# Kernel tuning notes

Hardware: AMD Instinct MI355X
Metric: run time of the kernel (lower is better)

Reference implementation:

```python
import jax, jax.numpy as jnp
import numpy as np

N, E, D, T = 50000, 800000, 64, 4
FI = D // T   # per-tower input features (divide_input=True)
FO = D // T   # per-tower output features (output_dim // towers)
NAGG, NSC = 4, 3  # mean/min/max/std ; identity/amplification/attenuation
AVG_LOG = float(np.log(17.0))  # from deg histogram: all nodes have degree 16


def setup_inputs() -> dict:
    key = jax.random.key(0)
    ks = jax.random.split(key, 12)
    rn = lambda k, s: jax.random.normal(k, s, dtype=jnp.float32) * 0.1
    z = lambda s: jnp.zeros(s, jnp.float32)
    post_in = (1 + NAGG * NSC) * FI  # cat([x, scaled aggregations]) per tower
    return {
        "x": jax.random.normal(ks[0], (N, D), dtype=jnp.float32),
        "edge_index": jax.random.randint(ks[1], (2, E), 0, N),
        "alpha": jnp.full((1,), 0.5, dtype=jnp.float32),
        "lin_self_W": rn(ks[2], (D, D)), "lin_self_b": z((D,)),
        "pre_W_s2d": rn(ks[3], (T, 2 * FI, FI)), "pre_b_s2d": z((T, FI)),
        "post_W_s2d": rn(ks[4], (T, post_in, FO)), "post_b_s2d": z((T, FO)),
        "lin_W_s2d": rn(ks[5], (T * FO, D)), "lin_b_s2d": z((D,)),
        "pre_W_d2s": rn(ks[6], (T, 2 * FI, FI)), "pre_b_d2s": z((T, FI)),
        "post_W_d2s": rn(ks[7], (T, post_in, FO)), "post_b_d2s": z((T, FO)),
        "lin_W_d2s": rn(ks[8], (T * FO, D)), "lin_b_d2s": z((D,)),
    }


def _pna(x, recv, send, preW, preb, postW, postb, linW, linb):
    """One PNAConv: messages from `send` nodes aggregated at `recv` nodes."""
    n = x.shape[0]
    xt = x.reshape(n, T, FI)
    # message: per tower cat(x_i, x_j) -> single pre layer (pre_layers=1)
    h = jnp.concatenate([xt[recv], xt[send]], axis=-1)          # [E, T, 2*FI]
    m = jnp.einsum('etf,tfg->etg', h, preW) + preb              # [E, T, FI]
    # aggregators: mean, min, max, std (scatter-reduce over receiver)
    cnt = jax.ops.segment_sum(jnp.ones((recv.shape[0],), m.dtype), recv, n)
    deg = jnp.maximum(cnt, 1.0)[:, None, None]                  # clamp(1), as PyG
    mean = jax.ops.segment_sum(m, recv, n) / deg
    mean_sq = jax.ops.segment_sum(m * m, recv, n) / deg
    std = jnp.sqrt(jnp.maximum(mean_sq - mean * mean, 0.0) + 1e-5)
    has = (cnt > 0.0)[:, None, None]
    mn = jnp.where(has, jax.ops.segment_min(m, recv, n), 0.0)
    mx = jnp.where(has, jax.ops.segment_max(m, recv, n), 0.0)
    agg = jnp.concatenate([mean, mn, mx, std], axis=-1)         # [n, T, 4*FI]
    # degree scalers: identity, amplification, attenuation
    amp = jnp.log(deg + 1.0) / AVG_LOG
    out = jnp.concatenate([agg, agg * amp, agg / amp], axis=-1)  # [n, T, 12*FI]
    out = jnp.concatenate([xt, out], axis=-1)                   # [n, T, 13*FI]
    out = jnp.einsum('ntf,tfg->ntg', out, postW) + postb        # [n, T, FO]
    return out.reshape(n, T * FO) @ linW + linb                 # [n, D]


def reference(x, edge_index, alpha, lin_self_W, lin_self_b,
              pre_W_s2d, pre_b_s2d, post_W_s2d, post_b_s2d, lin_W_s2d, lin_b_s2d,
              pre_W_d2s, pre_b_d2s, post_W_d2s, post_b_d2s, lin_W_d2s, lin_b_d2s):
    src, dst = edge_index[0], edge_index[1]
    y_self = x @ lin_self_W + lin_self_b
    # flow='source_to_target': x_j = src, aggregated at dst
    y_s2d = _pna(x, dst, src, pre_W_s2d, pre_b_s2d, post_W_s2d, post_b_s2d, lin_W_s2d, lin_b_s2d)
    # flow='target_to_source': x_j = dst, aggregated at src
    y_d2s = _pna(x, src, dst, pre_W_d2s, pre_b_d2s, post_W_d2s, post_b_d2s, lin_W_d2s, lin_b_d2s)
    a = alpha[0]
    return y_self + (1.0 - a) * y_s2d + a * y_d2s
```

## Files before the change

kernel.cpp:

```cpp
#include <hip/hip_runtime.h>
#include <math.h>


typedef _Float16 half_t;
typedef __attribute__((ext_vector_type(8))) _Float16 half8;
typedef __attribute__((ext_vector_type(2))) _Float16 half2v;
typedef __attribute__((ext_vector_type(4))) float f32x4;

#define FCAP 12288

static __device__ __forceinline__ unsigned pkmin(unsigned a, unsigned b) {
    unsigned r;
    asm("v_pk_min_f16 %0, %1, %2" : "=v"(r) : "v"(a), "v"(b));
    return r;
}
static __device__ __forceinline__ unsigned pkmax(unsigned a, unsigned b) {
    unsigned r;
    asm("v_pk_max_f16 %0, %1, %2" : "=v"(r) : "v"(a), "v"(b));
    return r;
}
static __device__ __forceinline__ int h2i(half2v h) { return __builtin_bit_cast(int, h); }
static __device__ __forceinline__ half2v i2h(int i) { return __builtin_bit_cast(half2v, i); }
static __device__ __forceinline__ half2v u2h(unsigned i) { return __builtin_bit_cast(half2v, i); }
static __device__ __forceinline__ half2v pkrtz(float a, float b) {
    return __builtin_bit_cast(half2v, __builtin_amdgcn_cvt_pkrtz(a, b));
}

__global__ __launch_bounds__(256) void k_pre(
    const int* __restrict__ ei, int nE, int nN,
    int* __restrict__ histD, int* __restrict__ histS,
    const float* __restrict__ postW1, const float* __restrict__ postW2,
    const float* __restrict__ linW1, const float* __restrict__ linW2,
    const float* __restrict__ Wself, const float* __restrict__ bself,
    const float* __restrict__ linb1, const float* __restrict__ linb2,
    const float* __restrict__ postb1, const float* __restrict__ postb2,
    const float* __restrict__ alpha,
    half_t* __restrict__ WLg, half_t* __restrict__ WfinTg, float* __restrict__ bfin,
    const float* __restrict__ x,
    const float* __restrict__ preW1, const float* __restrict__ preW2,
    const float* __restrict__ preb1, const float* __restrict__ preb2,
    half_t* __restrict__ P1, half_t* __restrict__ P2,
    half_t* __restrict__ Q1, half_t* __restrict__ Q2, half_t* __restrict__ xh) {
    int tid = threadIdx.x;
    int b = blockIdx.x;
    if (b < 256) {
        __shared__ int hD[256], hS[256];
        hD[tid] = 0; hS[tid] = 0;
        __syncthreads();
        int chunk = (nE + 255) >> 8;
        int lo = b * chunk;
        int hi = lo + chunk; if (hi > nE) hi = nE;
        for (int e = lo + tid; e < hi; e += 256) {
            int s = ei[e], d = ei[nE + e];
            atomicAdd(&hD[d >> 8], 1);
            atomicAdd(&hS[s >> 8], 1);
        }
        __syncthreads();
        histD[tid * 256 + b] = hD[tid];
        histS[tid * 256 + b] = hS[tid];
    } else if (b < 320) {
        const float a = alpha[0];
        int id = (b - 256) * 256 + tid;
        const int stride = 64 * 256;
        for (int i = id; i < 24 * 16 * 72; i += stride) {
            int m = i / (16 * 72);
            int r = i % (16 * 72);
            int go = r / 72, k = r % 72;
            int d = m / 12, t = (m / 3) % 4, mat = m % 3;
            float v = 0.f;
            if (k < 64) {
                int stat = k >> 4, g = k & 15;
                int basep = (mat == 0) ? 1 : (mat == 1 ? 5 : 9);
                const float* pw = d ? postW2 : postW1;
                v = pw[t * 3328 + ((basep + stat) * 16 + g) * 16 + go];
            }
            WLg[i] = (half_t)v;
        }
        for (int i = id; i < 64 * 192; i += stride) {
            int o = i / 192, k = i % 192;
            float v;
            if (k < 64)       v = (1.f - a) * linW1[k * 64 + o];
            else if (k < 128) v = a * linW2[(k - 64) * 64 + o];
            else {
                int kx = k - 128, t = kx >> 4, f = kx & 15;
                v = Wself[kx * 64 + o];
                float s1 = 0.f, s2 = 0.f;
                for (int go = 0; go < 16; ++go) {
                    s1 += postW1[t * 3328 + f * 16 + go] * linW1[(t * 16 + go) * 64 + o];
                    s2 += postW2[t * 3328 + f * 16 + go] * linW2[(t * 16 + go) * 64 + o];
                }
                v += (1.f - a) * s1 + a * s2;
            }
            WfinTg[i] = (half_t)v;
        }
        for (int i = id; i < 64; i += stride) {
            float v = bself[i] + (1.f - a) * linb1[i] + a * linb2[i];
            for (int j = 0; j < 64; ++j)
                v += (1.f - a) * postb1[j] * linW1[j * 64 + i]
                   + a * postb2[j] * linW2[j * 64 + i];
            bfin[i] = v;
        }
    } else {
        int vb = b - 320;
        const int lane = tid & 63;
        const int t = lane >> 4, g = lane & 15;
        const int base = t << 4;
        float wsP1[16], wsP2[16], wsQ1[16], wsQ2[16];
#pragma unroll
        for (int f = 0; f < 16; ++f) {
            wsP1[f] = preW1[t * 512 + (16 + f) * 16 + g];
            wsP2[f] = preW2[t * 512 + (16 + f) * 16 + g];
            wsQ1[f] = preW1[t * 512 + f * 16 + g];
            wsQ2[f] = preW2[t * 512 + f * 16 + g];
        }
        const float pb1 = preb1[lane], pb2 = preb2[lane];
        int node = (vb * 256 + tid) >> 6;
        const int stride = (768 * 256) >> 6;
        for (; node < nN; node += stride) {
            float xv = x[(size_t)node * 64 + lane];
            float p1 = 0.f, p2 = 0.f, q1 = pb1, q2 = pb2;
#pragma unroll
            for (int f = 0; f < 16; ++f) {
                float v = __shfl(xv, base + f, 64);
                p1 = fmaf(v, wsP1[f], p1);
                p2 = fmaf(v, wsP2[f], p2);
                q1 = fmaf(v, wsQ1[f], q1);
                q2 = fmaf(v, wsQ2[f], q2);
            }
            size_t o = (size_t)node * 64 + lane;
            P1[o] = (half_t)p1;
            P2[o] = (half_t)p2;
            Q1[o] = (half_t)q1;
            Q2[o] = (half_t)q2;
            xh[o] = (half_t)xv;
        }
    }
}

__global__ __launch_bounds__(256) void k_scanA(
    const int* __restrict__ cnt0, const int* __restrict__ cnt1,
    int* __restrict__ off0, int* __restrict__ off1,
    int* __restrict__ bsum, int n, int nchunk) {
    int arr = blockIdx.x >= nchunk;
    int c = blockIdx.x - (arr ? nchunk : 0);
    const int* cnt = arr ? cnt1 : cnt0;
    int* off = arr ? off1 : off0;
    int tid = threadIdx.x;
    int base = c * 1024 + tid * 4;
    int v[4];
#pragma unroll
    for (int k = 0; k < 4; ++k) { int i = base + k; v[k] = (i < n) ? cnt[i] : 0; }
    int tsum = v[0] + v[1] + v[2] + v[3];
    int lane = tid & 63, wid = tid >> 6;
    int incl = tsum;
#pragma unroll
    for (int d = 1; d < 64; d <<= 1) {
        int t = __shfl_up(incl, d, 64);
        if (lane >= d) incl += t;
    }
    __shared__ int ws[4];
    if (lane == 63) ws[wid] = incl;
    __syncthreads();
    int wpre = 0;
    for (int ww = 0; ww < wid; ++ww) wpre += ws[ww];
    int e = wpre + incl - tsum;
#pragma unroll
    for (int k = 0; k < 4; ++k) { int i = base + k; if (i < n) off[i] = e; e += v[k]; }
    if (tid == 255) bsum[blockIdx.x] = wpre + incl;
}

__global__ __launch_bounds__(256) void k_scanB(
    int* __restrict__ off0, int* __restrict__ off1,
    const int* __restrict__ bsum, int n, int nchunk) {
    int arr = blockIdx.x >= nchunk;
    int c = blockIdx.x - (arr ? nchunk : 0);
    int* off = arr ? off1 : off0;
    const int* bs = bsum + (arr ? nchunk : 0);
    __shared__ int pre_s, tot_s;
    int tid = threadIdx.x;
    if (tid < 64) {
        int v = (tid < nchunk) ? bs[tid] : 0;
        int incl = v;
#pragma unroll
        for (int d = 1; d < 64; d <<= 1) {
            int t = __shfl_up(incl, d, 64);
            if (tid >= d) incl += t;
        }
        if (tid == c) pre_s = incl - v;
        if (tid == nchunk - 1) tot_s = incl;
    }
    __syncthreads();
    int pre = pre_s;
    int base = c * 1024 + tid * 4;
#pragma unroll
    for (int k = 0; k < 4; ++k) {
        int i = base + k;
        if (i < n) off[i] += pre;
    }
    if (c == 0 && tid == 0) off[n] = tot_s;
}

__global__ __launch_bounds__(256) void k_bin(
    const int* __restrict__ ei, int nE, int nbuck,
    const int* __restrict__ curD, const int* __restrict__ curS,
    unsigned* __restrict__ binnedD, unsigned* __restrict__ binnedS) {
    __shared__ int cD[256], cS[256];
    int tid = threadIdx.x;
    int hb = blockIdx.x;
    if (tid < nbuck) {
        cD[tid] = curD[tid * 256 + hb];
        cS[tid] = curS[tid * 256 + hb];
    }
    __syncthreads();
    int chunk = (nE + 255) >> 8;
    int lo = hb * chunk;
    int hi = lo + chunk; if (hi > nE) hi = nE;
    for (int e = lo + tid; e < hi; e += 256) {
        int s = ei[e], d = ei[nE + e];
        unsigned pk = (unsigned)s | ((unsigned)d << 16);
        int p = atomicAdd(&cD[d >> 8], 1);
        binnedD[p] = pk;
        int q = atomicAdd(&cS[s >> 8], 1);
        binnedS[q] = pk;
    }
}

__global__ __launch_bounds__(256) void k_fine(
    const unsigned* __restrict__ binnedD, const unsigned* __restrict__ binnedS,
    const int* __restrict__ curD, const int* __restrict__ curS,
    int* __restrict__ off_dst, int* __restrict__ off_src,
    unsigned short* __restrict__ adj_dst, unsigned short* __restrict__ adj_src,
    int nE, int nN, int nbuck) {
    int bk = blockIdx.x;
    int dd = 0;
    if (bk >= nbuck) { dd = 1; bk -= nbuck; }
    const unsigned* binned = dd ? binnedS : binnedD;
    const int* cur = dd ? curS : curD;
    int* off = dd ? off_src : off_dst;
    unsigned short* adj = dd ? adj_src : adj_dst;
    __shared__ int ncnt[256];
    __shared__ int cur2[256];
    __shared__ unsigned short stage[FCAP];
    int tid = threadIdx.x;
    ncnt[tid] = 0;
    __syncthreads();
    int base = cur[bk * 256];
    int endp = cur[(bk + 1) * 256];
    int cntE = endp - base;
    int n0 = bk << 8;
    for (int i = tid; i < cntE; i += 256) {
        unsigned pk = binned[base + i];
        int key = dd ? (int)(pk & 0xFFFFu) : (int)(pk >> 16);
        atomicAdd(&ncnt[key - n0], 1);
    }
    __syncthreads();
    if (tid < 64) {
        int i4 = tid << 2;
        int v0 = ncnt[i4], v1 = ncnt[i4 + 1], v2 = ncnt[i4 + 2], v3 = ncnt[i4 + 3];
        int tsum = v0 + v1 + v2 + v3;
        int incl = tsum;
#pragma unroll
        for (int d = 1; d < 64; d <<= 1) {
            int t = __shfl_up(incl, d, 64);
            if (tid >= d) incl += t;
        }
        int excl = incl - tsum;
        ncnt[i4] = excl;
        ncnt[i4 + 1] = excl + v0;
        ncnt[i4 + 2] = excl + v0 + v1;
        ncnt[i4 + 3] = excl + v0 + v1 + v2;
    }
    __syncthreads();
    cur2[tid] = ncnt[tid];
    int node = n0 + tid;
    if (node < nN) off[node] = base + ncnt[tid];
    if (bk == nbuck - 1 && tid == 0) off[nN] = nE;
    __syncthreads();
    for (int i = tid; i < cntE; i += 256) {
        unsigned pk = binned[base + i];
        int key = dd ? (int)(pk & 0xFFFFu) : (int)(pk >> 16);
        int oth = dd ? (int)(pk >> 16) : (int)(pk & 0xFFFFu);
        int pos = atomicAdd(&cur2[key - n0], 1);
        if (pos < FCAP) stage[pos] = (unsigned short)oth;
        else adj[base + pos] = (unsigned short)oth;
    }
    __syncthreads();
    int lim = cntE < FCAP ? cntE : FCAP;
    for (int i = tid; i < lim; i += 256) adj[base + i] = stage[i];
}

__global__ __launch_bounds__(256) void k_gather(
    const half_t* __restrict__ P1, const half_t* __restrict__ P2,
    const half_t* __restrict__ Q1, const half_t* __restrict__ Q2,
    const int* __restrict__ off1, const unsigned short* __restrict__ adj1,
    const int* __restrict__ off2, const unsigned short* __restrict__ adj2,
    half_t* __restrict__ agg1, half_t* __restrict__ agg2,
    float* __restrict__ amp1, float* __restrict__ ramp1,
    float* __restrict__ amp2, float* __restrict__ ramp2, int nN, int nE) {
    int tid = threadIdx.x;
    const int lane = tid & 63;
    const int grp = lane >> 4;
    const int fl = lane & 15;
    const int fl8 = fl << 3;
    int wstart = (blockIdx.x * blockDim.x + tid) >> 6;
    int wstride = (gridDim.x * blockDim.x) >> 6;
#pragma unroll
    for (int d = 0; d < 2; ++d) {
        const char* Pc = (const char*)(d ? P2 : P1);
        const char* Qc = (const char*)(d ? Q2 : Q1);
        const int* off = d ? off2 : off1;
        const unsigned short* adj = d ? adj2 : adj1;
        char* aggc = (char*)(d ? agg2 : agg1);
        float* ampA = d ? amp2 : amp1;
        float* rampA = d ? ramp2 : ramp1;
        for (int node = wstart; node < nN; node += wstride) {
            int beg = off[node], end = off[node + 1];
            int cnt = end - beg;
            int li = beg + lane;
            int adjv = adj[li < nE ? li : 0];
            half2v s01 = {(half_t)0, (half_t)0}, s23 = {(half_t)0, (half_t)0};
            half2v ss01 = {(half_t)0, (half_t)0}, ss23 = {(half_t)0, (half_t)0};
            unsigned mn0 = 0x7C007C00u, mn1 = 0x7C007C00u;
            unsigned mx0 = 0xFC00FC00u, mx1 = 0xFC00FC00u;
            int jm = (cnt < 64) ? (cnt & ~7) : 64;
            int j = 0;
            for (; j + 8 <= jm; j += 8) {
                int na = __shfl(adjv, j + grp, 64);
                int nb = __shfl(adjv, j + 4 + grp, 64);
                uint2 ua = *(const uint2*)(Pc + na * 128 + fl8);
                uint2 ub = *(const uint2*)(Pc + nb * 128 + fl8);
                half2v a0 = u2h(ua.x), a1 = u2h(ua.y);
                half2v b0 = u2h(ub.x), b1 = u2h(ub.y);
                s01 += a0 + b0; s23 += a1 + b1;
                ss01 += a0 * a0; ss23 += a1 * a1;
                ss01 += b0 * b0; ss23 += b1 * b1;
                mn0 = pkmin(mn0, pkmin(ua.x, ub.x));
                mn1 = pkmin(mn1, pkmin(ua.y, ub.y));
                mx0 = pkmax(mx0, pkmax(ua.x, ub.x));
                mx1 = pkmax(mx1, pkmax(ua.y, ub.y));
            }
            for (int jj = beg + j; jj < end; jj += 4) {
                int idx = jj + grp;
                if (idx < end) {
                    int nc = adj[idx];
                    uint2 uc = *(const uint2*)(Pc + nc * 128 + fl8);
                    half2v c0 = u2h(uc.x), c1 = u2h(uc.y);
                    s01 += c0; s23 += c1;
                    ss01 += c0 * c0; ss23 += c1 * c1;
                    mn0 = pkmin(mn0, uc.x); mn1 = pkmin(mn1, uc.y);
                    mx0 = pkmax(mx0, uc.x); mx1 = pkmax(mx1, uc.y);
                }
            }
#pragma unroll
            for (int sh = 16; sh <= 32; sh <<= 1) {
                s01 += i2h(__shfl_xor(h2i(s01), sh, 64));
                s23 += i2h(__shfl_xor(h2i(s23), sh, 64));
                ss01 += i2h(__shfl_xor(h2i(ss01), sh, 64));
                ss23 += i2h(__shfl_xor(h2i(ss23), sh, 64));
                mn0 = pkmin(mn0, (unsigned)__shfl_xor((int)mn0, sh, 64));
                mn1 = pkmin(mn1, (unsigned)__shfl_xor((int)mn1, sh, 64));
                mx0 = pkmax(mx0, (unsigned)__shfl_xor((int)mx0, sh, 64));
                mx1 = pkmax(mx1, (unsigned)__shfl_xor((int)mx1, sh, 64));
            }
            float deg = (cnt > 0) ? (float)cnt : 1.0f;
            float inv = 1.0f / deg;
            float se0 = (float)s01[0], se1 = (float)s01[1];
            float se2 = (float)s23[0], se3 = (float)s23[1];
            float sq0 = (float)ss01[0], sq1 = (float)ss01[1];
            float sq2 = (float)ss23[0], sq3 = (float)ss23[1];
            float me0 = se0 * inv, me1 = se1 * inv, me2 = se2 * inv, me3 = se3 * inv;
            float st0 = sqrtf(fmaxf(fmaf(-me0, me0, sq0 * inv), 0.f) + 1e-5f);
            float st1 = sqrtf(fmaxf(fmaf(-me1, me1, sq1 * inv), 0.f) + 1e-5f);
            float st2 = sqrtf(fmaxf(fmaf(-me2, me2, sq2 * inv), 0.f) + 1e-5f);
            float st3 = sqrtf(fmaxf(fmaf(-me3, me3, sq3 * inv), 0.f) + 1e-5f);
            uint2 qu = *(const uint2*)(Qc + node * 128 + fl8);
            half2v q01 = u2h(qu.x), q23 = u2h(qu.y);
            half2v hm01, hm23, hl01, hl23, hh01, hh23;
            if (cnt > 0) {
                hm01 = q01 + pkrtz(me0, me1);
                hm23 = q23 + pkrtz(me2, me3);
                hl01 = q01 + u2h(mn0); hl23 = q23 + u2h(mn1);
                hh01 = q01 + u2h(mx0); hh23 = q23 + u2h(mx1);
            } else {
                half2v z = {(half_t)0, (half_t)0};
                hm01 = z; hm23 = z; hl01 = z; hl23 = z; hh01 = z; hh23 = z;
            }
            half2v hs01 = pkrtz(st0, st1);
            half2v hs23 = pkrtz(st2, st3);
            if (lane < 16) {
                char* ab = aggc + (size_t)node * 512 + (fl >> 2) * 128 + (fl & 3) * 8;
                uint2 w0; w0.x = (unsigned)h2i(hm01); w0.y = (unsigned)h2i(hm23);
                uint2 w1; w1.x = (unsigned)h2i(hl01); w1.y = (unsigned)h2i(hl23);
                uint2 w2; w2.x = (unsigned)h2i(hh01); w2.y = (unsigned)h2i(hh23);
                uint2 w3; w3.x = (unsigned)h2i(hs01); w3.y = (unsigned)h2i(hs23);
                *(uint2*)(ab)      = w0;
                *(uint2*)(ab + 32) = w1;
                *(uint2*)(ab + 64) = w2;
                *(uint2*)(ab + 96) = w3;
            }
            if (lane == 0) {
                float ampv = __log2f(deg + 1.0f) * 0.24465054f;
                ampA[node] = ampv;
                rampA[node] = 1.0f / ampv;
            }
        }
    }
}

__global__ __launch_bounds__(256, 2) void k_c(
    const half_t* __restrict__ xh,
    const half_t* __restrict__ agg1, const half_t* __restrict__ agg2,
    const float* __restrict__ amp1, const float* __restrict__ ramp1,
    const float* __restrict__ amp2, const float* __restrict__ ramp2,
    const half_t* __restrict__ WLg, const half_t* __restrict__ WfinT,
    const float* __restrict__ bfin, float* __restrict__ out, int nN) {
    __shared__ half_t WLs[24 * 16 * 72];
    __shared__ half_t osb[4 * 16 * 72];
    int tid = threadIdx.x;
    {
        const uint4* src = (const uint4*)WLg;
        uint4* dst = (uint4*)WLs;
        for (int i = tid; i < (24 * 16 * 72) / 8; i += 256) dst[i] = src[i];
    }
    __syncthreads();
    int w = tid >> 6, lane = tid & 63;
    int l15 = lane & 15, g4 = lane >> 4;
    half_t* ow = osb + w * (16 * 72) + l15 * 72;
    half8 wfr[4][6];
#pragma unroll
    for (int ct = 0; ct < 4; ++ct)
#pragma unroll
        for (int kk = 0; kk < 6; ++kk)
            wfr[ct][kk] = *(const half8*)(WfinT + (ct * 16 + l15) * 192 + kk * 32 + g4 * 8);
    float4 bf4[4];
#pragma unroll
    for (int ct = 0; ct < 4; ++ct)
        bf4[ct] = *(const float4*)(bfin + ct * 16 + g4 * 4);
    int nwaves = gridDim.x * 4;
    int wgid = blockIdx.x * 4 + w;
    int ntiles = (nN + 15) >> 4;
    for (int tile = wgid; tile < ntiles; tile += nwaves) {
        int nrow = (tile << 4) + l15;
        int nrowc = (nrow < nN) ? nrow : (nN - 1);
        half8 xbf[2];
#pragma unroll
        for (int ks = 0; ks < 2; ++ks)
            xbf[ks] = *(const half8*)(xh + (size_t)nrowc * 64 + ks * 32 + g4 * 8);
        f32x4 accY[4] = {{0,0,0,0},{0,0,0,0},{0,0,0,0},{0,0,0,0}};
#pragma unroll
        for (int d = 0; d < 2; ++d) {
            const half_t* agg = d ? agg2 : agg1;
            float ampv = (d ? amp2 : amp1)[nrowc];
            float rampv = (d ? ramp2 : ramp1)[nrowc];
#pragma unroll
            for (int t = 0; t < 4; ++t) {
                half8 b0 = *(const half8*)(agg + (size_t)nrowc * 256 + t * 64 + g4 * 8);
                half8 b1 = *(const half8*)(agg + (size_t)nrowc * 256 + t * 64 + 32 + g4 * 8);
                const half_t* wb = WLs + ((d * 12 + t * 3) * 16 + l15) * 72 + g4 * 8;
                half8 aA0 = *(const half8*)(wb);
                half8 aA1 = *(const half8*)(wb + 32);
                half8 aB0 = *(const half8*)(wb + 16 * 72);
                half8 aB1 = *(const half8*)(wb + 16 * 72 + 32);
                half8 aE0 = *(const half8*)(wb + 32 * 72);
                half8 aE1 = *(const half8*)(wb + 32 * 72 + 32);
                f32x4 zA = {0,0,0,0}, zB = {0,0,0,0}, zE = {0,0,0,0};
                zA = __builtin_amdgcn_mfma_f32_16x16x32_f16(aA0, b0, zA, 0, 0, 0);
                zA = __builtin_amdgcn_mfma_f32_16x16x32_f16(aA1, b1, zA, 0, 0, 0);
                zB = __builtin_amdgcn_mfma_f32_16x16x32_f16(aB0, b0, zB, 0, 0, 0);
                zB = __builtin_amdgcn_mfma_f32_16x16x32_f16(aB1, b1, zB, 0, 0, 0);
                zE = __builtin_amdgcn_mfma_f32_16x16x32_f16(aE0, b0, zE, 0, 0, 0);
                zE = __builtin_amdgcn_mfma_f32_16x16x32_f16(aE1, b1, zE, 0, 0, 0);
                float o0 = zA[0] + ampv * zB[0] + rampv * zE[0];
                float o1 = zA[1] + ampv * zB[1] + rampv * zE[1];
                float o2 = zA[2] + ampv * zB[2] + rampv * zE[2];
                float o3 = zA[3] + ampv * zB[3] + rampv * zE[3];
                half2v p0; p0[0] = (half_t)o0; p0[1] = (half_t)o1;
                half2v p1; p1[0] = (half_t)o2; p1[1] = (half_t)o3;
                *(half2v*)(ow + t * 16 + g4 * 4) = p0;
                *(half2v*)(ow + t * 16 + g4 * 4 + 2) = p1;
            }
#pragma unroll
            for (int ks = 0; ks < 2; ++ks) {
                half8 ob = *(const half8*)(ow + ks * 32 + g4 * 8);
#pragma unroll
                for (int ct = 0; ct < 4; ++ct)
                    accY[ct] = __builtin_amdgcn_mfma_f32_16x16x32_f16(wfr[ct][d * 2 + ks], ob, accY[ct], 0, 0, 0);
            }
        }
#pragma unroll
        for (int ks = 0; ks < 2; ++ks)
#pragma unroll
            for (int ct = 0; ct < 4; ++ct)
                accY[ct] = __builtin_amdgcn_mfma_f32_16x16x32_f16(wfr[ct][4 + ks], xbf[ks], accY[ct], 0, 0, 0);
        if (nrow < nN) {
#pragma unroll
            for (int ct = 0; ct < 4; ++ct) {
                float4 st;
                st.x = accY[ct][0] + bf4[ct].x;
                st.y = accY[ct][1] + bf4[ct].y;
                st.z = accY[ct][2] + bf4[ct].z;
                st.w = accY[ct][3] + bf4[ct].w;
                *(float4*)(out + (size_t)nrow * 64 + ct * 16 + g4 * 4) = st;
            }
        }
    }
}

extern "C" void kernel_launch(void* const* d_in, const int* in_sizes, int n_in,
                              void* d_out, int out_size, void* d_ws, size_t ws_size,
                              hipStream_t stream) {
    const float* x      = (const float*)d_in[0];
    const int*   ei     = (const int*)d_in[1];
    const float* alpha  = (const float*)d_in[2];
    const float* Wself  = (const float*)d_in[3];
    const float* bself  = (const float*)d_in[4];
    const float* preW1  = (const float*)d_in[5];
    const float* preb1  = (const float*)d_in[6];
    const float* postW1 = (const float*)d_in[7];
    const float* postb1 = (const float*)d_in[8];
    const float* linW1  = (const float*)d_in[9];
    const float* linb1  = (const float*)d_in[10];
    const float* preW2  = (const float*)d_in[11];
    const float* preb2  = (const float*)d_in[12];
    const float* postW2 = (const float*)d_in[13];
    const float* postb2 = (const float*)d_in[14];
    const float* linW2  = (const float*)d_in[15];
    const float* linb2  = (const float*)d_in[16];
    float* out = (float*)d_out;
    const int nN = in_sizes[0] / 64;
    const int nE = in_sizes[1] / 2;
    const int nbuck = (nN + 255) >> 8;
    const int nH = nbuck * 256;
    const int nchunk = (nH + 1023) >> 10;

    char* w = (char*)d_ws;
    size_t ofs = 0;
    auto alloc = [&](size_t bytes) {
        char* p = w + ofs;
        ofs = (ofs + bytes + 255) & ~(size_t)255;
        return p;
    };
    half_t* P1   = (half_t*)alloc((size_t)nN * 64 * 2);
    half_t* P2   = (half_t*)alloc((size_t)nN * 64 * 2);
    half_t* Q1   = (half_t*)alloc((size_t)nN * 64 * 2);
    half_t* Q2   = (half_t*)alloc((size_t)nN * 64 * 2);
    half_t* xh   = (half_t*)alloc((size_t)nN * 64 * 2);
    half_t* agg1 = (half_t*)alloc((size_t)nN * 256 * 2);
    half_t* agg2 = (half_t*)alloc((size_t)nN * 256 * 2);
    float* amp1  = (float*)alloc((size_t)nN * 4);
    float* ramp1 = (float*)alloc((size_t)nN * 4);
    float* amp2  = (float*)alloc((size_t)nN * 4);
    float* ramp2 = (float*)alloc((size_t)nN * 4);
    half_t* WLg   = (half_t*)alloc(24 * 16 * 72 * 2);
    half_t* WfinT = (half_t*)alloc(64 * 192 * 2);
    float* bfin   = (float*)alloc(64 * 4);
    int* histD = (int*)alloc(256 * 256 * 4);
    int* histS = (int*)alloc(256 * 256 * 4);
    int* curD  = (int*)alloc((256 * 256 + 1) * 4);
    int* curS  = (int*)alloc((256 * 256 + 1) * 4);
    unsigned* binnedD = (unsigned*)alloc((size_t)nE * 4);
    unsigned* binnedS = (unsigned*)alloc((size_t)nE * 4);
    int* off_dst = (int*)alloc((size_t)(nN + 1) * 4);
    int* off_src = (int*)alloc((size_t)(nN + 1) * 4);
    unsigned short* adj_dst = (unsigned short*)alloc((size_t)nE * 2);
    unsigned short* adj_src = (unsigned short*)alloc((size_t)nE * 2);
    int* bsum = (int*)alloc(2 * 64 * 4);

    k_pre<<<1088, 256, 0, stream>>>(ei, nE, nN, histD, histS,
                                    postW1, postW2, linW1, linW2, Wself, bself,
                                    linb1, linb2, postb1, postb2, alpha,
                                    WLg, WfinT, bfin,
                                    x, preW1, preW2, preb1, preb2,
                                    P1, P2, Q1, Q2, xh);
    k_scanA<<<2 * nchunk, 256, 0, stream>>>(histD, histS, curD, curS, bsum, nH, nchunk);
    k_scanB<<<2 * nchunk, 256, 0, stream>>>(curD, curS, bsum, nH, nchunk);
    k_bin<<<256, 256, 0, stream>>>(ei, nE, nbuck, curD, curS, binnedD, binnedS);
    k_fine<<<2 * nbuck, 256, 0, stream>>>(binnedD, binnedS, curD, curS,
                                          off_dst, off_src, adj_dst, adj_src,
                                          nE, nN, nbuck);
    k_gather<<<2048, 256, 0, stream>>>(P1, P2, Q1, Q2, off_dst, adj_dst, off_src, adj_src,
                                       agg1, agg2, amp1, ramp1, amp2, ramp2, nN, nE);
    k_c<<<512, 256, 0, stream>>>(xh, agg1, agg2, amp1, ramp1, amp2, ramp2,
                                 WLg, WfinT, bfin, out, nN);
}
```

Measured before the change: 156.7 us.

## Map one node per 16-lane group in gather instead of one node per wavefront

The gather kernel now processes four nodes per wavefront, with each 16-lane quarter walking one node's full adjacency list serially and unrolled by four. This removes the cross-group shuffle reductions and the adjacency broadcast through shuffles, and every lane now does useful stores. In exchange each group issues more dependent serial loads per node (16 edges), and adjacency indices are loaded redundantly by all 16 lanes of a group.

```diff
diff --git a/kernel.cpp b/kernel.cpp
--- a/kernel.cpp
+++ b/kernel.cpp
@@ -20,7 +20,6 @@
     return r;
 }
 static __device__ __forceinline__ int h2i(half2v h) { return __builtin_bit_cast(int, h); }
-static __device__ __forceinline__ half2v i2h(int i) { return __builtin_bit_cast(half2v, i); }
 static __device__ __forceinline__ half2v u2h(unsigned i) { return __builtin_bit_cast(half2v, i); }
 static __device__ __forceinline__ half2v pkrtz(float a, float b) {
     return __builtin_bit_cast(half2v, __builtin_amdgcn_cvt_pkrtz(a, b));
@@ -299,11 +298,12 @@
     float* __restrict__ amp2, float* __restrict__ ramp2, int nN, int nE) {
     int tid = threadIdx.x;
     const int lane = tid & 63;
-    const int grp = lane >> 4;
+    const int g = lane >> 4;
     const int fl = lane & 15;
     const int fl8 = fl << 3;
-    int wstart = (blockIdx.x * blockDim.x + tid) >> 6;
-    int wstride = (gridDim.x * blockDim.x) >> 6;
+    int w4 = (blockIdx.x * 256 + tid) >> 6;
+    int wstride = (gridDim.x * 256) >> 6;
+    int ngroups = (nN + 3) >> 2;
 #pragma unroll
     for (int d = 0; d < 2; ++d) {
         const char* Pc = (const char*)(d ? P2 : P1);
@@ -313,54 +313,49 @@
         char* aggc = (char*)(d ? agg2 : agg1);
         float* ampA = d ? amp2 : amp1;
         float* rampA = d ? ramp2 : ramp1;
-        for (int node = wstart; node < nN; node += wstride) {
-            int beg = off[node], end = off[node + 1];
+        for (int gi = w4; gi < ngroups; gi += wstride) {
+            int node = gi * 4 + g;
+            bool act = node < nN;
+            int nodec = act ? node : (nN - 1);
+            int beg = off[nodec], end = off[nodec + 1];
             int cnt = end - beg;
-            int li = beg + lane;
-            int adjv = adj[li < nE ? li : 0];
             half2v s01 = {(half_t)0, (half_t)0}, s23 = {(half_t)0, (half_t)0};
             half2v ss01 = {(half_t)0, (half_t)0}, ss23 = {(half_t)0, (half_t)0};
             unsigned mn0 = 0x7C007C00u, mn1 = 0x7C007C00u;
             unsigned mx0 = 0xFC00FC00u, mx1 = 0xFC00FC00u;
-            int jm = (cnt < 64) ? (cnt & ~7) : 64;
-            int j = 0;
-            for (; j + 8 <= jm; j += 8) {
-                int na = __shfl(adjv, j + grp, 64);
-                int nb = __shfl(adjv, j + 4 + grp, 64);
-                uint2 ua = *(const uint2*)(Pc + na * 128 + fl8);
-                uint2 ub = *(const uint2*)(Pc + nb * 128 + fl8);
-                half2v a0 = u2h(ua.x), a1 = u2h(ua.y);
-                half2v b0 = u2h(ub.x), b1 = u2h(ub.y);
-                s01 += a0 + b0; s23 += a1 + b1;
+            int j = beg;
+            for (; j + 4 <= end; j += 4) {
+                int n0 = adj[j + 0];
+                int n1 = adj[j + 1];
+                int n2 = adj[j + 2];
+                int n3 = adj[j + 3];
+                uint2 u0 = *(const uint2*)(Pc + n0 * 128 + fl8);
+                uint2 u1 = *(const uint2*)(Pc + n1 * 128 + fl8);
+                uint2 u2 = *(const uint2*)(Pc + n2 * 128 + fl8);
+                uint2 u3 = *(const uint2*)(Pc + n3 * 128 + fl8);
+                half2v a0 = u2h(u0.x), a1 = u2h(u0.y);
+                half2v b0 = u2h(u1.x), b1 = u2h(u1.y);
+                half2v c0 = u2h(u2.x), c1 = u2h(u2.y);
+                half2v e0 = u2h(u3.x), e1 = u2h(u3.y);
+                s01 += (a0 + b0) + (c0 + e0);
+                s23 += (a1 + b1) + (c1 + e1);
                 ss01 += a0 * a0; ss23 += a1 * a1;
                 ss01 += b0 * b0; ss23 += b1 * b1;
-                mn0 = pkmin(mn0, pkmin(ua.x, ub.x));
-                mn1 = pkmin(mn1, pkmin(ua.y, ub.y));
-                mx0 = pkmax(mx0, pkmax(ua.x, ub.x));
-                mx1 = pkmax(mx1, pkmax(ua.y, ub.y));
-            }
-            for (int jj = beg + j; jj < end; jj += 4) {
-                int idx = jj + grp;
-                if (idx < end) {
-                    int nc = adj[idx];
-                    uint2 uc = *(const uint2*)(Pc + nc * 128 + fl8);
-                    half2v c0 = u2h(uc.x), c1 = u2h(uc.y);
-                    s01 += c0; s23 += c1;
-                    ss01 += c0 * c0; ss23 += c1 * c1;
-                    mn0 = pkmin(mn0, uc.x); mn1 = pkmin(mn1, uc.y);
-                    mx0 = pkmax(mx0, uc.x); mx1 = pkmax(mx1, uc.y);
-                }
-            }
-#pragma unroll
-            for (int sh = 16; sh <= 32; sh <<= 1) {
-                s01 += i2h(__shfl_xor(h2i(s01), sh, 64));
-                s23 += i2h(__shfl_xor(h2i(s23), sh, 64));
-                ss01 += i2h(__shfl_xor(h2i(ss01), sh, 64));
-                ss23 += i2h(__shfl_xor(h2i(ss23), sh, 64));
-                mn0 = pkmin(mn0, (unsigned)__shfl_xor((int)mn0, sh, 64));
-                mn1 = pkmin(mn1, (unsigned)__shfl_xor((int)mn1, sh, 64));
-                mx0 = pkmax(mx0, (unsigned)__shfl_xor((int)mx0, sh, 64));
-                mx1 = pkmax(mx1, (unsigned)__shfl_xor((int)mx1, sh, 64));
+                ss01 += c0 * c0; ss23 += c1 * c1;
+                ss01 += e0 * e0; ss23 += e1 * e1;
+                mn0 = pkmin(mn0, pkmin(pkmin(u0.x, u1.x), pkmin(u2.x, u3.x)));
+                mn1 = pkmin(mn1, pkmin(pkmin(u0.y, u1.y), pkmin(u2.y, u3.y)));
+                mx0 = pkmax(mx0, pkmax(pkmax(u0.x, u1.x), pkmax(u2.x, u3.x)));
+                mx1 = pkmax(mx1, pkmax(pkmax(u0.y, u1.y), pkmax(u2.y, u3.y)));
+            }
+            for (; j < end; ++j) {
+                int n0 = adj[j];
+                uint2 u0 = *(const uint2*)(Pc + n0 * 128 + fl8);
+                half2v a0 = u2h(u0.x), a1 = u2h(u0.y);
+                s01 += a0; s23 += a1;
+                ss01 += a0 * a0; ss23 += a1 * a1;
+                mn0 = pkmin(mn0, u0.x); mn1 = pkmin(mn1, u0.y);
+                mx0 = pkmax(mx0, u0.x); mx1 = pkmax(mx1, u0.y);
             }
             float deg = (cnt > 0) ? (float)cnt : 1.0f;
             float inv = 1.0f / deg;
@@ -373,7 +368,7 @@
             float st1 = sqrtf(fmaxf(fmaf(-me1, me1, sq1 * inv), 0.f) + 1e-5f);
             float st2 = sqrtf(fmaxf(fmaf(-me2, me2, sq2 * inv), 0.f) + 1e-5f);
             float st3 = sqrtf(fmaxf(fmaf(-me3, me3, sq3 * inv), 0.f) + 1e-5f);
-            uint2 qu = *(const uint2*)(Qc + node * 128 + fl8);
+            uint2 qu = *(const uint2*)(Qc + nodec * 128 + fl8);
             half2v q01 = u2h(qu.x), q23 = u2h(qu.y);
             half2v hm01, hm23, hl01, hl23, hh01, hh23;
             if (cnt > 0) {
@@ -387,7 +382,7 @@
             }
             half2v hs01 = pkrtz(st0, st1);
             half2v hs23 = pkrtz(st2, st3);
-            if (lane < 16) {
+            if (act) {
                 char* ab = aggc + (size_t)node * 512 + (fl >> 2) * 128 + (fl & 3) * 8;
                 uint2 w0; w0.x = (unsigned)h2i(hm01); w0.y = (unsigned)h2i(hm23);
                 uint2 w1; w1.x = (unsigned)h2i(hl01); w1.y = (unsigned)h2i(hl23);
@@ -397,11 +392,11 @@
                 *(uint2*)(ab + 32) = w1;
                 *(uint2*)(ab + 64) = w2;
                 *(uint2*)(ab + 96) = w3;
-            }
-            if (lane == 0) {
-                float ampv = __log2f(deg + 1.0f) * 0.24465054f;
-                ampA[node] = ampv;
-                rampA[node] = 1.0f / ampv;
+                if (fl == 0) {
+                    float ampv = __log2f(deg + 1.0f) * 0.24465054f;
+                    ampA[node] = ampv;
+                    rampA[node] = 1.0f / ampv;
+                }
             }
         }
     }
```

Result: faster. 138.7 us (-11.5%).
